# Performance work log

Measured on AMD Instinct MI355X. Metric: run time of the kernel, lower is better.

Reference implementation:

```python
import jax, jax.numpy as jnp
import numpy as np

B, S, D, E, K = 4, 2048, 768, 8, 2


def setup_inputs() -> dict:
    key = jax.random.key(0)
    ks = jax.random.split(key, 5)
    s = 0.02
    return {
        "x": jax.random.normal(ks[0], (B, S, D), dtype=jnp.float32),
        "gate_w": jax.random.normal(ks[1], (D, E), dtype=jnp.float32) * s,
        "gate_b": jnp.zeros((E,), dtype=jnp.float32),
        "w1": jax.random.normal(ks[2], (E, D, D), dtype=jnp.float32) * s,
        "b1": jnp.zeros((E, D), dtype=jnp.float32),
        "w2": jax.random.normal(ks[3], (E, D, D), dtype=jnp.float32) * s,
        "b2": jnp.zeros((E, D), dtype=jnp.float32),
    }


def reference(x, gate_w, gate_b, w1, b1, w2, b2):
    # MoE forward, eval mode (no gate noise, dropout = identity)
    b, s, d = x.shape
    xf = x.reshape(-1, d)                                  # [T, D]
    T = xf.shape[0]

    gate_logits = xf @ gate_w + gate_b                     # [T, E]
    gate_scores = jax.nn.softmax(gate_logits, axis=-1)

    topv, topi = jax.lax.top_k(gate_scores, K)             # [T, K]
    topv = topv / (jnp.sum(topv, axis=-1, keepdims=True) + 1e-8)

    # scatter top-k weights into dense per-expert combine weights [T, E]
    comb = jnp.zeros((T, E), dtype=xf.dtype).at[
        jnp.arange(T)[:, None], topi].add(topv)

    # expert MLPs (dense over experts; combine weights zero-out unselected)
    h = jax.nn.relu(jnp.einsum('td,edh->teh', xf, w1) + b1)  # [T, E, D]
    y = jnp.einsum('teh,eho->teo', h, w2) + b2               # [T, E, D]
    out = jnp.einsum('te,teo->to', comb, y).reshape(b, s, -1)

    # load-balance aux loss (CV^2 of expert importance)
    importance = gate_scores.sum(axis=0)                   # [E]
    cv2 = importance.var() / (importance.mean() ** 2 + 1e-8)
    aux_loss = 0.01 * cv2
    return out, aux_loss
```

## Files before the change

### kernel.cpp

```cpp
#include <hip/hip_runtime.h>


#define T_TOK 8192
#define D_DIM 768
#define E_EXP 8
#define TK    16384

typedef __attribute__((ext_vector_type(4))) float f32x4;
typedef __attribute__((ext_vector_type(8))) short s16x8;
typedef __attribute__((ext_vector_type(8))) unsigned short u16x8;

static __device__ __forceinline__ unsigned short f2bf(float f) {
    union { float f; unsigned u; } v; v.f = f;
    unsigned r = v.u + 0x7FFFu + ((v.u >> 16) & 1u);
    return (unsigned short)(r >> 16);
}
static __device__ __forceinline__ float bf2f(unsigned short h) {
    union { unsigned u; float f; } v; v.u = ((unsigned)h) << 16;
    return v.f;
}

static __device__ __forceinline__ void gload_lds16(const unsigned short* g, unsigned short* l) {
    __builtin_amdgcn_global_load_lds(
        (const __attribute__((address_space(1))) unsigned int*)(const void*)g,
        (__attribute__((address_space(3))) unsigned int*)(void*)l,
        16, 0, 0);
}

__global__ __launch_bounds__(256) void gate_kernel(
    const float* __restrict__ x, const float* __restrict__ gw,
    const float* __restrict__ gb, unsigned short* __restrict__ xb,
    int* __restrict__ ea, int* __restrict__ eb,
    float* __restrict__ wa, float* __restrict__ wb,
    int* __restrict__ counts, float* __restrict__ importance,
    int* __restrict__ basep, int* __restrict__ cursor,
    int* __restrict__ done, float* __restrict__ aux_out)
{
    __shared__ float s_imp[4][8];
    __shared__ int   s_cnt[4][8];
    const int tid = threadIdx.x, wid = tid >> 6, lane = tid & 63;
    const int wg = blockIdx.x * 4 + wid;

    float imp[8]; int cnt[8];
    #pragma unroll
    for (int e = 0; e < 8; ++e) { imp[e] = 0.f; cnt[e] = 0; }

    for (int i = 0; i < 8; ++i) {
        const int t = wg + i * 1024;
        const float* xr = x + (size_t)t * D_DIM;
        float xv[12];
        float acc[8];
        #pragma unroll
        for (int e = 0; e < 8; ++e) acc[e] = 0.f;
        #pragma unroll
        for (int j = 0; j < 12; ++j) {
            const int d = lane + j * 64;
            float v = xr[d];
            xv[j] = v;
            xb[(size_t)t * D_DIM + d] = f2bf(v);
        }
        #pragma unroll
        for (int j = 0; j < 12; ++j) {
            const int d = lane + j * 64;
            const f32x4* g = (const f32x4*)(gw + (size_t)d * 8);
            f32x4 g0 = g[0], g1 = g[1];
            float v = xv[j];
            acc[0] += v * g0[0]; acc[1] += v * g0[1];
            acc[2] += v * g0[2]; acc[3] += v * g0[3];
            acc[4] += v * g1[0]; acc[5] += v * g1[1];
            acc[6] += v * g1[2]; acc[7] += v * g1[3];
        }
        #pragma unroll
        for (int s = 1; s < 64; s <<= 1) {
            #pragma unroll
            for (int e = 0; e < 8; ++e) acc[e] += __shfl_xor(acc[e], s);
        }
        float lg[8], mx = -1e30f;
        #pragma unroll
        for (int e = 0; e < 8; ++e) { lg[e] = acc[e] + gb[e]; mx = fmaxf(mx, lg[e]); }
        float p[8], ssum = 0.f;
        #pragma unroll
        for (int e = 0; e < 8; ++e) { p[e] = expf(lg[e] - mx); ssum += p[e]; }
        float sc[8];
        float inv_s = 1.f / ssum;
        #pragma unroll
        for (int e = 0; e < 8; ++e) { sc[e] = p[e] * inv_s; imp[e] += sc[e]; }
        int i0 = 0;
        #pragma unroll
        for (int e = 1; e < 8; ++e) if (sc[e] > sc[i0]) i0 = e;
        int i1 = (i0 == 0) ? 1 : 0;
        #pragma unroll
        for (int e = 0; e < 8; ++e) if (e != i0 && sc[e] > sc[i1]) i1 = e;
        float v0 = sc[i0], v1 = sc[i1];
        float inv = 1.f / (v0 + v1 + 1e-8f);
        if (lane == 0) {
            ea[t] = i0; eb[t] = i1; wa[t] = v0 * inv; wb[t] = v1 * inv;
            cnt[i0]++; cnt[i1]++;
        }
    }
    if (lane == 0) {
        #pragma unroll
        for (int e = 0; e < 8; ++e) { s_imp[wid][e] = imp[e]; s_cnt[wid][e] = cnt[e]; }
    }
    __syncthreads();
    if (tid < 8) {
        float si = 0.f; int sc2 = 0;
        #pragma unroll
        for (int w = 0; w < 4; ++w) { si += s_imp[w][tid]; sc2 += s_cnt[w][tid]; }
        atomicAdd(importance + tid, si);
        atomicAdd(counts + tid, sc2);
    }
    __threadfence();
    __syncthreads();
    if (tid == 0) {
        if (atomicAdd(done, 1) == (int)gridDim.x - 1) {
            int c[8]; float im[8];
            #pragma unroll
            for (int e = 0; e < 8; ++e) {
                c[e]  = atomicAdd(counts + e, 0);
                im[e] = atomicAdd(importance + e, 0.0f);
            }
            int b = 0;
            #pragma unroll
            for (int e = 0; e < 8; ++e) { basep[e] = b; cursor[e] = b; b += c[e]; }
            float mean = 0.f;
            #pragma unroll
            for (int e = 0; e < 8; ++e) mean += im[e];
            mean *= 0.125f;
            float var = 0.f;
            #pragma unroll
            for (int e = 0; e < 8; ++e) { float d = im[e] - mean; var += d * d; }
            var *= 0.125f;
            aux_out[0] = 0.01f * var / (mean * mean + 1e-8f);
        }
    }
}

__global__ __launch_bounds__(256) void scatter_kernel(
    const int* __restrict__ ea, const int* __restrict__ eb,
    const float* __restrict__ wa, const float* __restrict__ wb,
    int* __restrict__ cursor, int* __restrict__ list,
    float* __restrict__ wgt, int* __restrict__ slot)
{
    const int t = blockIdx.x * 256 + threadIdx.x;
    const int lane = threadIdx.x & 63;
    #pragma unroll
    for (int k = 0; k < 2; ++k) {
        const int e = k ? eb[t] : ea[t];
        const float w = k ? wb[t] : wa[t];
        int pos = 0;
        for (int ex = 0; ex < 8; ++ex) {
            unsigned long long m = __ballot(e == ex);
            if (e == ex) {
                int leader = __ffsll((unsigned long long)m) - 1;
                int n = __popcll(m);
                int p0 = 0;
                if (lane == leader) p0 = atomicAdd(cursor + ex, n);
                p0 = __shfl(p0, leader);
                pos = p0 + __popcll(m & ((1ull << lane) - 1ull));
            }
        }
        list[pos] = t; wgt[pos] = w; slot[t * 2 + k] = pos;
    }
}

__global__ __launch_bounds__(256) void tconv_kernel(
    const float* __restrict__ w1, const float* __restrict__ w2,
    unsigned short* __restrict__ w1t, unsigned short* __restrict__ w2t)
{
    const int z = blockIdx.z;
    const float* src = (z < 8 ? w1 : w2) + (size_t)(z & 7) * D_DIM * D_DIM;
    unsigned short* dst = (z < 8 ? w1t : w2t) + (size_t)(z & 7) * D_DIM * D_DIM;
    __shared__ float tile[32][33];
    const int tx = threadIdx.x, ty = threadIdx.y;
    const int k0 = blockIdx.x * 32, n0 = blockIdx.y * 32;
    #pragma unroll
    for (int j = 0; j < 4; ++j)
        tile[ty + j * 8][tx] = src[(size_t)(k0 + ty + j * 8) * D_DIM + n0 + tx];
    __syncthreads();
    #pragma unroll
    for (int j = 0; j < 4; ++j)
        dst[(size_t)(n0 + ty + j * 8) * D_DIM + k0 + tx] = f2bf(tile[tx][ty + j * 8]);
}

template<int GATHER, int RELU>
__global__ __launch_bounds__(256) void moe_gemm_kernel(
    const unsigned short* __restrict__ A, const unsigned short* __restrict__ Bt,
    const float* __restrict__ bias, unsigned short* __restrict__ C,
    const int* __restrict__ counts, const int* __restrict__ basep,
    const int* __restrict__ list)
{
    const int e = blockIdx.z;
    const int count = counts[e];
    const int m0 = blockIdx.x * 128;
    if (m0 >= count) return;
    const int n0 = blockIdx.y * 128;
    const int base = basep[e];

    __shared__ unsigned short Al[128 * 32];
    __shared__ unsigned short Bl[128 * 32];

    const int tid = threadIdx.x;
    const int lane = tid & 63, wid = tid >> 6;
    const int wr = wid >> 1, wc = wid & 1;

    const int sr = wid * 16 + (lane >> 2);
    const int sc = (lane & 3) * 8;

    int r0 = m0 + sr;      if (r0 >= count) r0 = count - 1;
    int r1 = m0 + 64 + sr; if (r1 >= count) r1 = count - 1;
    const size_t t0 = GATHER ? (size_t)list[base + r0] : (size_t)(base + r0);
    const size_t t1 = GATHER ? (size_t)list[base + r1] : (size_t)(base + r1);
    const unsigned short* gA0 = A + t0 * D_DIM + sc;
    const unsigned short* gA1 = A + t1 * D_DIM + sc;
    const unsigned short* gB0 = Bt + ((size_t)e * D_DIM + n0 + sr) * D_DIM + sc;
    const unsigned short* gB1 = Bt + ((size_t)e * D_DIM + n0 + 64 + sr) * D_DIM + sc;
    unsigned short* lA0 = &Al[(wid * 16) * 32];
    unsigned short* lA1 = &Al[(64 + wid * 16) * 32];
    unsigned short* lB0 = &Bl[(wid * 16) * 32];
    unsigned short* lB1 = &Bl[(64 + wid * 16) * 32];

    f32x4 acc[4][4];
    #pragma unroll
    for (int mi = 0; mi < 4; ++mi)
        #pragma unroll
        for (int ni = 0; ni < 4; ++ni)
            acc[mi][ni] = (f32x4)(0.f);

    for (int k0 = 0; k0 < D_DIM; k0 += 32) {
        __syncthreads();
        gload_lds16(gA0 + k0, lA0);
        gload_lds16(gA1 + k0, lA1);
        gload_lds16(gB0 + k0, lB0);
        gload_lds16(gB1 + k0, lB1);
        __syncthreads();

        s16x8 af[4], bf[4];
        #pragma unroll
        for (int mi = 0; mi < 4; ++mi)
            af[mi] = *(const s16x8*)&Al[(wr * 64 + mi * 16 + (lane & 15)) * 32 + (lane >> 4) * 8];
        #pragma unroll
        for (int ni = 0; ni < 4; ++ni)
            bf[ni] = *(const s16x8*)&Bl[(wc * 64 + ni * 16 + (lane & 15)) * 32 + (lane >> 4) * 8];
        #pragma unroll
        for (int mi = 0; mi < 4; ++mi)
            #pragma unroll
            for (int ni = 0; ni < 4; ++ni)
                acc[mi][ni] = __builtin_amdgcn_mfma_f32_16x16x32_bf16(
                    af[mi], bf[ni], acc[mi][ni], 0, 0, 0);
    }

    #pragma unroll
    for (int ni = 0; ni < 4; ++ni) {
        const int cn = n0 + wc * 64 + ni * 16 + (lane & 15);
        const float bv = bias[e * D_DIM + cn];
        #pragma unroll
        for (int mi = 0; mi < 4; ++mi) {
            #pragma unroll
            for (int j = 0; j < 4; ++j) {
                const int rm = m0 + wr * 64 + mi * 16 + (lane >> 4) * 4 + j;
                if (rm < count) {
                    float v = acc[mi][ni][j] + bv;
                    if (RELU) v = fmaxf(v, 0.f);
                    C[(size_t)(base + rm) * D_DIM + cn] = f2bf(v);
                }
            }
        }
    }
}

__global__ __launch_bounds__(256) void combine_kernel(
    const unsigned short* __restrict__ y, const int* __restrict__ slot,
    const float* __restrict__ wgt, float* __restrict__ out)
{
    const int g = blockIdx.x * 256 + threadIdx.x;
    const int t = g / 96;
    const int n = (g % 96) * 8;
    const int s0 = slot[t * 2], s1 = slot[t * 2 + 1];
    const float w0 = wgt[s0], w1 = wgt[s1];
    u16x8 ya = *(const u16x8*)(y + (size_t)s0 * D_DIM + n);
    u16x8 yb = *(const u16x8*)(y + (size_t)s1 * D_DIM + n);
    f32x4 o0, o1;
    #pragma unroll
    for (int i = 0; i < 4; ++i) o0[i] = w0 * bf2f(ya[i])     + w1 * bf2f(yb[i]);
    #pragma unroll
    for (int i = 0; i < 4; ++i) o1[i] = w0 * bf2f(ya[4 + i]) + w1 * bf2f(yb[4 + i]);
    float* op = out + (size_t)t * D_DIM + n;
    *(f32x4*)op       = o0;
    *(f32x4*)(op + 4) = o1;
}

extern "C" void kernel_launch(void* const* d_in, const int* in_sizes, int n_in,
                              void* d_out, int out_size, void* d_ws, size_t ws_size,
                              hipStream_t stream)
{
    const float* x  = (const float*)d_in[0];
    const float* gw = (const float*)d_in[1];
    const float* gb = (const float*)d_in[2];
    const float* w1 = (const float*)d_in[3];
    const float* b1 = (const float*)d_in[4];
    const float* w2 = (const float*)d_in[5];
    const float* b2 = (const float*)d_in[6];
    float* out = (float*)d_out;

    char* ws = (char*)d_ws;
    size_t off = 0;
    auto alloc = [&](size_t bytes) {
        char* p = ws + off; off += (bytes + 255) & ~(size_t)255; return p;
    };
    unsigned short* xb  = (unsigned short*)alloc((size_t)T_TOK * D_DIM * 2);
    unsigned short* w1t = (unsigned short*)alloc((size_t)E_EXP * D_DIM * D_DIM * 2);
    unsigned short* w2t = (unsigned short*)alloc((size_t)E_EXP * D_DIM * D_DIM * 2);
    unsigned short* h   = (unsigned short*)alloc((size_t)TK * D_DIM * 2);
    unsigned short* y   = (unsigned short*)alloc((size_t)TK * D_DIM * 2);
    int*   list = (int*)alloc(TK * 4);
    float* wgt  = (float*)alloc(TK * 4);
    int*   slot = (int*)alloc(TK * 4);
    int*   ea   = (int*)alloc(T_TOK * 4);
    int*   eb   = (int*)alloc(T_TOK * 4);
    float* wa   = (float*)alloc(T_TOK * 4);
    float* wb   = (float*)alloc(T_TOK * 4);
    int*   meta = (int*)alloc(256);
    int*   counts = meta;
    int*   basep  = meta + 8;
    int*   cursor = meta + 16;
    int*   done   = meta + 24;
    float* importance = (float*)(meta + 32);

    hipMemsetAsync(meta, 0, 256, stream);
    tconv_kernel<<<dim3(24, 24, 16), dim3(32, 8), 0, stream>>>(w1, w2, w1t, w2t);
    gate_kernel<<<256, 256, 0, stream>>>(x, gw, gb, xb, ea, eb, wa, wb, counts, importance,
                                         basep, cursor, done, out + (out_size - 1));
    scatter_kernel<<<32, 256, 0, stream>>>(ea, eb, wa, wb, cursor, list, wgt, slot);
    moe_gemm_kernel<1, 1><<<dim3(64, 6, 8), 256, 0, stream>>>(xb, w1t, b1, h, counts, basep, list);
    moe_gemm_kernel<0, 0><<<dim3(64, 6, 8), 256, 0, stream>>>(h, w2t, b2, y, counts, basep, list);
    combine_kernel<<<3072, 256, 0, stream>>>(y, slot, wgt, out);
}
```

Measured before the change: 305.9 us.

## Triple-buffer LDS in MoE GEMM and simplify top-2 selection

Replaces the single-buffered K loop in the expert GEMM with a three-stage LDS ring. Tile t+2 is issued via global_load_lds while tile t is consumed, and explicit vmcnt waits plus raw s_barrier replace the two __syncthreads per iteration, so global loads can overlap MFMA work. The gating kernel's top-2 search becomes a single pass and the per-expert counts are updated branchlessly in every lane. The cost is triple the LDS footprint, which may lower occupancy, and reliance on hand-tuned waitcnt ordering to stay correct.

```diff
diff --git a/kernel.cpp b/kernel.cpp
--- a/kernel.cpp
+++ b/kernel.cpp
@@ -85,17 +85,18 @@
         float inv_s = 1.f / ssum;
         #pragma unroll
         for (int e = 0; e < 8; ++e) { sc[e] = p[e] * inv_s; imp[e] += sc[e]; }
-        int i0 = 0;
-        #pragma unroll
-        for (int e = 1; e < 8; ++e) if (sc[e] > sc[i0]) i0 = e;
-        int i1 = (i0 == 0) ? 1 : 0;
-        #pragma unroll
-        for (int e = 0; e < 8; ++e) if (e != i0 && sc[e] > sc[i1]) i1 = e;
-        float v0 = sc[i0], v1 = sc[i1];
+        float v0 = sc[0], v1 = -1e30f;
+        int   i0 = 0,     i1 = -1;
+        #pragma unroll
+        for (int e = 1; e < 8; ++e) {
+            if (sc[e] > v0)      { v1 = v0; i1 = i0; v0 = sc[e]; i0 = e; }
+            else if (sc[e] > v1) { v1 = sc[e]; i1 = e; }
+        }
+        #pragma unroll
+        for (int e = 0; e < 8; ++e) cnt[e] += (e == i0 ? 1 : 0) + (e == i1 ? 1 : 0);
         float inv = 1.f / (v0 + v1 + 1e-8f);
         if (lane == 0) {
             ea[t] = i0; eb[t] = i1; wa[t] = v0 * inv; wb[t] = v1 * inv;
-            cnt[i0]++; cnt[i1]++;
         }
     }
     if (lane == 0) {
@@ -197,8 +198,11 @@
     const int n0 = blockIdx.y * 128;
     const int base = basep[e];
 
-    __shared__ unsigned short Al[128 * 32];
-    __shared__ unsigned short Bl[128 * 32];
+    constexpr int NT = D_DIM / 32;
+    constexpr int LB = 128 * 32;
+
+    __shared__ unsigned short Al[3 * LB];
+    __shared__ unsigned short Bl[3 * LB];
 
     const int tid = threadIdx.x;
     const int lane = tid & 63, wid = tid >> 6;
@@ -215,10 +219,8 @@
     const unsigned short* gA1 = A + t1 * D_DIM + sc;
     const unsigned short* gB0 = Bt + ((size_t)e * D_DIM + n0 + sr) * D_DIM + sc;
     const unsigned short* gB1 = Bt + ((size_t)e * D_DIM + n0 + 64 + sr) * D_DIM + sc;
-    unsigned short* lA0 = &Al[(wid * 16) * 32];
-    unsigned short* lA1 = &Al[(64 + wid * 16) * 32];
-    unsigned short* lB0 = &Bl[(wid * 16) * 32];
-    unsigned short* lB1 = &Bl[(64 + wid * 16) * 32];
+    const int lds0 = (wid * 16) * 32;
+    const int lds1 = (64 + wid * 16) * 32;
 
     f32x4 acc[4][4];
     #pragma unroll
@@ -227,28 +229,47 @@
         for (int ni = 0; ni < 4; ++ni)
             acc[mi][ni] = (f32x4)(0.f);
 
-    for (int k0 = 0; k0 < D_DIM; k0 += 32) {
-        __syncthreads();
-        gload_lds16(gA0 + k0, lA0);
-        gload_lds16(gA1 + k0, lA1);
-        gload_lds16(gB0 + k0, lB0);
-        gload_lds16(gB1 + k0, lB1);
-        __syncthreads();
-
-        s16x8 af[4], bf[4];
+#define STAGE(kt, bi) do {                                   \
+        const int _k = (kt) * 32;                            \
+        gload_lds16(gA0 + _k, Al + (bi) * LB + lds0);        \
+        gload_lds16(gA1 + _k, Al + (bi) * LB + lds1);        \
+        gload_lds16(gB0 + _k, Bl + (bi) * LB + lds0);        \
+        gload_lds16(gB1 + _k, Bl + (bi) * LB + lds1);        \
+    } while (0)
+
+    STAGE(0, 0);
+    STAGE(1, 1);
+    asm volatile("s_waitcnt vmcnt(4)" ::: "memory");
+    __builtin_amdgcn_s_barrier();
+    __builtin_amdgcn_sched_barrier(0);
+
+    #pragma unroll
+    for (int t = 0; t < NT; ++t) {
+        const int cb = t % 3;
+        const int sb = (t + 2) % 3;
+        if (t + 2 < NT) STAGE(t + 2, sb);
+
+        s16x8 af[4], bfr[4];
         #pragma unroll
         for (int mi = 0; mi < 4; ++mi)
-            af[mi] = *(const s16x8*)&Al[(wr * 64 + mi * 16 + (lane & 15)) * 32 + (lane >> 4) * 8];
+            af[mi] = *(const s16x8*)&Al[cb * LB + (wr * 64 + mi * 16 + (lane & 15)) * 32 + (lane >> 4) * 8];
         #pragma unroll
         for (int ni = 0; ni < 4; ++ni)
-            bf[ni] = *(const s16x8*)&Bl[(wc * 64 + ni * 16 + (lane & 15)) * 32 + (lane >> 4) * 8];
+            bfr[ni] = *(const s16x8*)&Bl[cb * LB + (wc * 64 + ni * 16 + (lane & 15)) * 32 + (lane >> 4) * 8];
         #pragma unroll
         for (int mi = 0; mi < 4; ++mi)
             #pragma unroll
             for (int ni = 0; ni < 4; ++ni)
                 acc[mi][ni] = __builtin_amdgcn_mfma_f32_16x16x32_bf16(
-                    af[mi], bf[ni], acc[mi][ni], 0, 0, 0);
-    }
+                    af[mi], bfr[ni], acc[mi][ni], 0, 0, 0);
+
+        __builtin_amdgcn_sched_barrier(0);
+        if (t + 2 < NT) { asm volatile("s_waitcnt vmcnt(4)" ::: "memory"); }
+        else            { asm volatile("s_waitcnt vmcnt(0)" ::: "memory"); }
+        __builtin_amdgcn_s_barrier();
+        __builtin_amdgcn_sched_barrier(0);
+    }
+#undef STAGE
 
     #pragma unroll
     for (int ni = 0; ni < 4; ++ni) {
```

Measured after the change: 309.5 us. About the same (+1.2%).
